# Kernel optimization log

Measured on AMD Instinct MI355X. Metric: run time of the kernel, lower is better.

Reference implementation:

```python
import jax, jax.numpy as jnp
import numpy as np

B, DIM, H, W = 1, 96, 192, 192
HEADS = 6
HD = DIM // HEADS
WIN = (8, 4)
STRIDE = (4, 2)
WH, WW = WIN
N = WH * WW
SCALE = HD ** -0.5
EPS = 1e-8

_hs = np.arange(0, H - WH + 1, STRIDE[0])
_ws = np.arange(0, W - WW + 1, STRIDE[1])
NH, NW = len(_hs), len(_ws)
HIDX = jnp.asarray(_hs[:, None] + np.arange(WH)[None, :])  # (NH, WH)
WIDX = jnp.asarray(_ws[:, None] + np.arange(WW)[None, :])  # (NW, WW)

# relative-position index table (N, N)
_co = np.stack(np.meshgrid(np.arange(WH), np.arange(WW), indexing='ij')).reshape(2, -1)
_rp = _co[:, :, None] - _co[:, None, :]
_rp[0] += WH - 1
_rp[1] += WW - 1
_rp[0] *= 2 * WW - 1
REL_IDX = jnp.asarray(_rp[0] + _rp[1])


def _clin(wr, wi, x):
    # complex 1x1 conv as channel matmul
    xr, xi = x.real, x.imag
    yr = jnp.einsum('oc,nchw->nohw', wr, xr) - jnp.einsum('oc,nchw->nohw', wi, xi)
    yi = jnp.einsum('oc,nchw->nohw', wr, xi) + jnp.einsum('oc,nchw->nohw', wi, xr)
    return jax.lax.complex(yr, yi)


def _bn(x, g, b):
    # BatchNorm2d in training mode: batch statistics, biased variance, eps=1e-5
    mu = x.mean(axis=(0, 2, 3), keepdims=True)
    var = ((x - mu) ** 2).mean(axis=(0, 2, 3), keepdims=True)
    return g[None, :, None, None] * (x - mu) * jax.lax.rsqrt(var + 1e-5) + b[None, :, None, None]


def _cbn(x, gr, br, gi, bi):
    return jax.lax.complex(_bn(x.real, gr, br), _bn(x.imag, gi, bi))


def _cgelu(x):
    mag = jnp.abs(x)
    return x * (jax.nn.gelu(mag, approximate=False) / (mag + EPS))


def _heads(t):
    # (Bn, H*D, wh, ww) -> (Bn, H, N, D)
    return t.reshape(-1, HEADS, HD, N).transpose(0, 1, 3, 2)


def reference(x_real, x_imag, qkv_wr, qkv_wi, proj_wr, proj_wi, rel,
              mlp1_wr, mlp1_wi, mlp2_wr, mlp2_wi,
              n1_gr, n1_br, n1_gi, n1_bi, n2_gr, n2_br, n2_gi, n2_bi):
    x = jax.lax.complex(x_real, x_imag)  # (B, C, H, W)

    # unfold: gather overlapping windows -> (B, C, NH, NW, WH, WW)
    xw = x[:, :, HIDX[:, None, :, None], WIDX[None, :, None, :]]
    xw = xw.transpose(0, 2, 3, 1, 4, 5).reshape(B * NH * NW, DIM, WH, WW)

    qkv = _clin(qkv_wr, qkv_wi, xw)
    q, k, v = jnp.split(qkv, 3, axis=1)
    q, k, v = _heads(q), _heads(k), _heads(v)

    attn = jnp.einsum('bhnd,bhmd->bhnm', q, jnp.conj(k)) * SCALE
    bias = rel[:, REL_IDX]  # (HEADS, N, N), real
    attn = attn + bias[None]
    mag = jnp.abs(attn)
    wsm = jax.nn.softmax(mag, axis=-1)
    attn = attn * (wsm / (mag + EPS))  # magnitude-softmax, phase preserved
    out = jnp.einsum('bhnm,bhmd->bhnd', attn, v)
    out = out.transpose(0, 1, 3, 2).reshape(-1, DIM, WH, WW)
    out = _clin(proj_wr, proj_wi, out)

    # fold: scatter-add windows back, then overlap-average
    out = out.reshape(B, NH, NW, DIM, WH, WW).transpose(0, 3, 1, 2, 4, 5)
    folded = jnp.zeros((B, DIM, H, W), jnp.complex64).at[
        :, :, HIDX[:, None, :, None], WIDX[None, :, None, :]].add(out)
    counts = jnp.zeros((H, W), jnp.float32).at[
        HIDX[:, None, :, None], WIDX[None, :, None, :]].add(1.0)
    x_ = folded / (counts + EPS)

    x = _cbn(x + x_, n1_gr, n1_br, n1_gi, n1_bi)
    m = _clin(mlp2_wr, mlp2_wi, _cgelu(_clin(mlp1_wr, mlp1_wi, x)))
    x = _cbn(x + m, n2_gr, n2_br, n2_gi, n2_bi)
    return jnp.stack([x.real, x.imag], axis=0)  # (2, B, C, H, W)


def setup_inputs() -> dict:
    key = jax.random.key(0)
    ks = jax.random.split(key, 11)
    n = lambda k, s: jax.random.normal(k, s, jnp.float32) * 0.02
    return {
        'x_real': jax.random.normal(ks[0], (B, DIM, H, W), jnp.float32),
        'x_imag': jax.random.normal(ks[1], (B, DIM, H, W), jnp.float32),
        'qkv_wr': n(ks[2], (3 * DIM, DIM)), 'qkv_wi': n(ks[3], (3 * DIM, DIM)),
        'proj_wr': n(ks[4], (DIM, DIM)), 'proj_wi': n(ks[5], (DIM, DIM)),
        'rel': n(ks[6], (HEADS, (2 * WH - 1) * (2 * WW - 1))),
        'mlp1_wr': n(ks[7], (4 * DIM, DIM)), 'mlp1_wi': n(ks[8], (4 * DIM, DIM)),
        'mlp2_wr': n(ks[9], (DIM, 4 * DIM)), 'mlp2_wi': n(ks[10], (DIM, 4 * DIM)),
        'n1_gr': jnp.ones(DIM), 'n1_br': jnp.zeros(DIM),
        'n1_gi': jnp.ones(DIM), 'n1_bi': jnp.zeros(DIM),
        'n2_gr': jnp.ones(DIM), 'n2_br': jnp.zeros(DIM),
        'n2_gi': jnp.ones(DIM), 'n2_bi': jnp.zeros(DIM),
    }
```

## Files before the change

kernel.cpp:

```cpp
#include <hip/hip_runtime.h>
#include <math.h>

#define PIX 36864
#define IMW 192
#define NWIN 4465
#define NWIN_W 95
#define NTASK (NWIN * 6)

typedef short bf16x8 __attribute__((ext_vector_type(8)));
typedef short bf16x4 __attribute__((ext_vector_type(4)));
typedef float floatx4 __attribute__((ext_vector_type(4)));

#if defined(__has_builtin)
#  if __has_builtin(__builtin_amdgcn_rcpf)
#    define RCP(x) __builtin_amdgcn_rcpf(x)
#  endif
#endif
#ifndef RCP
#  define RCP(x) (1.0f / (x))
#endif

__device__ __forceinline__ unsigned short f2bf(float f) {
    union { float f; unsigned u; } v; v.f = f;
    unsigned r = v.u + 0x7fff + ((v.u >> 16) & 1);
    return (unsigned short)(r >> 16);
}
__device__ __forceinline__ float bf2f(unsigned short b) {
    union { unsigned u; float f; } v; v.u = ((unsigned)b) << 16;
    return v.f;
}

__device__ __forceinline__ void emit3(
    const float* __restrict__ wr, const float* __restrict__ wi,
    unsigned short* __restrict__ outr, unsigned short* __restrict__ outi,
    unsigned short* __restrict__ outni, int e)
{
    outr[e] = f2bf(wr[e]);
    unsigned short b = f2bf(wi[e]);
    outi[e]  = b;
    outni[e] = b ^ 0x8000;
}

__global__ __launch_bounds__(256) void prep_kernel(
    const float* __restrict__ qwr, const float* __restrict__ qwi,
    const float* __restrict__ pwr, const float* __restrict__ pwi,
    const float* __restrict__ w2r, const float* __restrict__ w2i,
    const float* __restrict__ xr,  const float* __restrict__ xi,
    unsigned short* __restrict__ wq, unsigned short* __restrict__ wp,
    unsigned short* __restrict__ w2, float* __restrict__ ssum,
    unsigned short* __restrict__ dr, unsigned short* __restrict__ di)
{
    int blk = blockIdx.x;
    if (blk < 108)      { emit3(qwr, qwi, wq, wq + 27648, wq + 55296, blk * 256 + threadIdx.x); return; }
    if (blk < 144)      { emit3(pwr, pwi, wp, wp + 9216,  wp + 18432, (blk - 108) * 256 + threadIdx.x); return; }
    if (blk < 288)      { emit3(w2r, w2i, w2, w2 + 36864, w2 + 73728, (blk - 144) * 256 + threadIdx.x); return; }
    if (blk == 288)     { for (int j = threadIdx.x; j < 768; j += 256) ssum[j] = 0.f; return; }
    int e  = blk - 289;
    int kb = e / 144;
    int n  = (e % 144) * 256 + threadIdx.x;
    bf16x8 vr, vi;
#pragma unroll
    for (int j = 0; j < 8; ++j) {
        ((unsigned short*)&vr)[j] = f2bf(xr[(size_t)(kb * 8 + j) * PIX + n]);
        ((unsigned short*)&vi)[j] = f2bf(xi[(size_t)(kb * 8 + j) * PIX + n]);
    }
    *(bf16x8*)&dr[((size_t)kb * PIX + n) * 8] = vr;
    *(bf16x8*)&di[((size_t)kb * PIX + n) * 8] = vi;
}

template<int K, int MT, int STORE>
__global__ __launch_bounds__(256, 2) void cgemm_mfma_kernel(
    const unsigned short* __restrict__ Wr, const unsigned short* __restrict__ Wi,
    const unsigned short* __restrict__ Wni,
    const unsigned short* __restrict__ Xr, const unsigned short* __restrict__ Xi,
    unsigned short* __restrict__ Pr, unsigned short* __restrict__ Pi, int N)
{
    const int lane = threadIdx.x & 63;
    const int wave = threadIdx.x >> 6;
    const int g = lane >> 4;
    const int r = lane & 15;
    const int m0 = (blockIdx.x % MT) * 32;
    const int n0 = (blockIdx.x / MT) * 256 + wave * 64;

    floatx4 accR[2][4], accI[2][4];
#pragma unroll
    for (int t = 0; t < 2; ++t)
#pragma unroll
        for (int j = 0; j < 4; ++j) {
            accR[t][j] = (floatx4){0.f, 0.f, 0.f, 0.f};
            accI[t][j] = (floatx4){0.f, 0.f, 0.f, 0.f};
        }

    for (int kc = 0; kc < K; kc += 32) {
        bf16x8 awr[2], awi[2], awni[2];
#pragma unroll
        for (int t = 0; t < 2; ++t) {
            size_t wb = (size_t)(m0 + t * 16 + r) * K + kc + g * 8;
            awr[t]  = *(const bf16x8*)&Wr[wb];
            awi[t]  = *(const bf16x8*)&Wi[wb];
            awni[t] = *(const bf16x8*)&Wni[wb];
        }
        bf16x8 bxr[4], bxi[4];
        const size_t krow = (size_t)((kc >> 3) + g);
#pragma unroll
        for (int j = 0; j < 4; ++j) {
            size_t off = (krow * N + n0 + j * 16 + r) * 8;
            bxr[j] = *(const bf16x8*)&Xr[off];
            bxi[j] = *(const bf16x8*)&Xi[off];
        }
#pragma unroll
        for (int t = 0; t < 2; ++t)
#pragma unroll
            for (int j = 0; j < 4; ++j) {
                accR[t][j] = __builtin_amdgcn_mfma_f32_16x16x32_bf16(awr[t],  bxr[j], accR[t][j], 0, 0, 0);
                accR[t][j] = __builtin_amdgcn_mfma_f32_16x16x32_bf16(awni[t], bxi[j], accR[t][j], 0, 0, 0);
                accI[t][j] = __builtin_amdgcn_mfma_f32_16x16x32_bf16(awr[t],  bxi[j], accI[t][j], 0, 0, 0);
                accI[t][j] = __builtin_amdgcn_mfma_f32_16x16x32_bf16(awi[t],  bxr[j], accI[t][j], 0, 0, 0);
            }
    }

    if (STORE == 3) {
#pragma unroll
        for (int t = 0; t < 2; ++t)
#pragma unroll
            for (int j = 0; j < 4; ++j) {
                int col = n0 + j * 16 + r;
#pragma unroll
                for (int reg = 0; reg < 4; ++reg) {
                    int row = m0 + t * 16 + g * 4 + reg;
                    Pr[(size_t)row * N + col] = f2bf(accR[t][j][reg]);
                    Pi[(size_t)row * N + col] = f2bf(accI[t][j][reg]);
                }
            }
    } else {
#pragma unroll
        for (int t = 0; t < 2; ++t) {
            int ch0 = m0 + t * 16;
            int which = ch0 / 96;
            int hh = (ch0 % 96) / 16;
#pragma unroll
            for (int j = 0; j < 4; ++j) {
                int col = n0 + j * 16 + r;
                bf16x4 pr, pi;
#pragma unroll
                for (int reg = 0; reg < 4; ++reg) {
                    ((unsigned short*)&pr)[reg] = f2bf(accR[t][j][reg]);
                    ((unsigned short*)&pi)[reg] = f2bf(accI[t][j][reg]);
                }
                size_t sb = (((size_t)col * 3 + which) * 6 + hh) * 32;
                *(bf16x4*)&Pr[sb + g * 4]      = pr;
                *(bf16x4*)&Pr[sb + 16 + g * 4] = pi;
            }
        }
    }
}

__global__ __launch_bounds__(256) void attn_mfma_kernel(
    const unsigned short* __restrict__ qkvb,
    const float* __restrict__ rel,
    unsigned short* __restrict__ wout)
{
    __shared__ unsigned aLDS[4][32 * 36];
    __shared__ unsigned vLDS[4][32 * 17];

    const int wv   = threadIdx.x >> 6;
    const int lane = threadIdx.x & 63;
    const int lr   = lane & 15;
    const int g    = lane >> 4;

    int t = blockIdx.x * 4 + wv;
    if (t >= NTASK) t = NTASK - 1;
    const int w = t / 6, h = t % 6;
    const int nh = w / NWIN_W, nw = w % NWIN_W;
    const int r0 = nh * 4, c0 = nw * 2;
    const int slot = ((nh & 1) << 1) | (nw & 1);

    unsigned* AL = aLDS[wv];
    unsigned* VL = vLDS[wv];

    auto slotq = [&](int p, int which) -> size_t {
        int gpix = (r0 + (p >> 2)) * IMW + c0 + (p & 3);
        return ((size_t)gpix * 18 + which * 6 + h) * 32;
    };

    {
        int m = lane & 31;
        int half = lane >> 5;
        size_t sv = slotq(m, 2);
        const bf16x8 vr = *(const bf16x8*)&qkvb[sv + half * 8];
        const bf16x8 vi = *(const bf16x8*)&qkvb[sv + 16 + half * 8];
#pragma unroll
        for (int j = 0; j < 8; ++j) {
            unsigned pk = (unsigned)(unsigned short)vr[j] |
                          ((unsigned)(unsigned short)vi[j] << 16);
            VL[m * 17 + half * 8 + j] = pk;
        }
    }

    const int hoff = (g >> 1) * 16;
    const int loff = (g & 1) * 8;
    const unsigned sm = (g >= 2) ? 0x80008000u : 0u;
    bf16x8 Are[2], Aim[2], Bre[2], Bim[2];
#pragma unroll
    for (int tt = 0; tt < 2; ++tt) {
        size_t sq = slotq(tt * 16 + lr, 0);
        size_t sk = slotq(tt * 16 + lr, 1);
        Are[tt] = *(const bf16x8*)&qkvb[sq + hoff + loff];
        Aim[tt] = *(const bf16x8*)&qkvb[sq + (16 - hoff) + loff];
        Bre[tt] = *(const bf16x8*)&qkvb[sk + hoff + loff];
        bf16x8 tmp = Bre[tt];
        unsigned* u = (unsigned*)&tmp;
        u[0] ^= sm; u[1] ^= sm; u[2] ^= sm; u[3] ^= sm;
        Bim[tt] = tmp;
    }

    const floatx4 z4 = (floatx4){0.f, 0.f, 0.f, 0.f};
    floatx4 Sre[2][2], Sim[2][2];
#pragma unroll
    for (int tn = 0; tn < 2; ++tn)
#pragma unroll
        for (int tm = 0; tm < 2; ++tm) {
            Sre[tn][tm] = __builtin_amdgcn_mfma_f32_16x16x32_bf16(Are[tn], Bre[tm], z4, 0, 0, 0);
            Sim[tn][tm] = __builtin_amdgcn_mfma_f32_16x16x32_bf16(Aim[tn], Bim[tm], z4, 0, 0, 0);
        }

    const float* relh = rel + h * 105;
#pragma unroll
    for (int tn = 0; tn < 2; ++tn)
#pragma unroll
        for (int tm = 0; tm < 2; ++tm) {
            int m = tm * 16 + lr;
            int ym = m >> 2, xm = m & 3;
            int yn = tn * 4 + g;
            int bidx = (yn - ym + 7) * 7 + (3 - xm);
#pragma unroll
            for (int reg = 0; reg < 4; ++reg) {
                float re = Sre[tn][tm][reg] * 0.25f + relh[bidx + reg];
                float im = Sim[tn][tm][reg] * 0.25f;
                int n = tn * 16 + g * 4 + reg;
                AL[n * 36 + m] = (unsigned)f2bf(re) | ((unsigned)f2bf(im) << 16);
            }
        }
    __syncthreads();

    {
        const int row = lane & 31;
        const int half = lane >> 5;
        unsigned* rp = &AL[row * 36 + half * 16];
        unsigned pk[16];
        *(uint4*)&pk[0]  = *(const uint4*)&rp[0];
        *(uint4*)&pk[4]  = *(const uint4*)&rp[4];
        *(uint4*)&pk[8]  = *(const uint4*)&rp[8];
        *(uint4*)&pk[12] = *(const uint4*)&rp[12];
        float re[16], im[16], mg[16];
#pragma unroll
        for (int j = 0; j < 16; ++j) {
            union { unsigned u; float f; } a, b;
            a.u = pk[j] << 16;
            b.u = pk[j] & 0xffff0000u;
            re[j] = a.f; im[j] = b.f;
            mg[j] = sqrtf(a.f * a.f + b.f * b.f);
        }
        float mx = mg[0];
#pragma unroll
        for (int j = 1; j < 16; ++j) mx = fmaxf(mx, mg[j]);
        mx = fmaxf(mx, __shfl_xor(mx, 32, 64));
        float es[16], ss = 0.f;
#pragma unroll
        for (int j = 0; j < 16; ++j) { es[j] = __expf(mg[j] - mx); ss += es[j]; }
        ss += __shfl_xor(ss, 32, 64);
        float inv = RCP(ss);
#pragma unroll
        for (int j = 0; j < 16; ++j) {
            float f = es[j] * inv * RCP(mg[j] + 1e-8f);
            pk[j] = (unsigned)f2bf(re[j] * f) | ((unsigned)f2bf(im[j] * f) << 16);
        }
        *(uint4*)&rp[0]  = *(uint4*)&pk[0];
        *(uint4*)&rp[4]  = *(uint4*)&pk[4];
        *(uint4*)&rp[8]  = *(uint4*)&pk[8];
        *(uint4*)&rp[12] = *(uint4*)&pk[12];
    }
    __syncthreads();

    floatx4 Pre[2] = {z4, z4}, Pim[2] = {z4, z4};
#pragma unroll
    for (int kc = 0; kc < 2; ++kc) {
        bf16x8 Bpr, Bpi;
        unsigned* bpr = (unsigned*)&Bpr;
        unsigned* bpi = (unsigned*)&Bpi;
#pragma unroll
        for (int p = 0; p < 4; ++p) {
            unsigned pv = VL[(kc * 16 + g * 4 + p) * 17 + lr];
            bpr[p] = pv ^ 0x80000000u;
            bpi[p] = (pv >> 16) | (pv << 16);
        }
#pragma unroll
        for (int tn = 0; tn < 2; ++tn) {
            bf16x8 Af = *(bf16x8*)&AL[(tn * 16 + lr) * 36 + kc * 16 + g * 4];
            Pre[tn] = __builtin_amdgcn_mfma_f32_16x16x32_bf16(Af, Bpr, Pre[tn], 0, 0, 0);
            Pim[tn] = __builtin_amdgcn_mfma_f32_16x16x32_bf16(Af, Bpi, Pim[tn], 0, 0, 0);
        }
    }

#pragma unroll
    for (int tn = 0; tn < 2; ++tn)
#pragma unroll
        for (int reg = 0; reg < 4; ++reg) {
            int n = tn * 16 + g * 4 + reg;
            int gpix = (r0 + (n >> 2)) * IMW + c0 + (n & 3);
            int ch = h * 16 + lr;
            unsigned pk = (unsigned)f2bf(Pre[tn][reg]) |
                          ((unsigned)f2bf(Pim[tn][reg]) << 16);
            *(unsigned*)&wout[(((size_t)gpix * 4 + slot) * 96 + ch) * 2] = pk;
        }
}

__global__ __launch_bounds__(256) void fold_pack_kernel(
    const unsigned short* __restrict__ wout,
    unsigned short* __restrict__ dr, unsigned short* __restrict__ di)
{
    int e = blockIdx.x * 256 + threadIdx.x;
    int gpix = e / 12;
    int kb   = e % 12;
    int r = gpix / IMW, c = gpix % IMW;
    int nh0 = (r >= 7) ? ((r - 4) >> 2) : 0;
    int nh1 = min(46, r >> 2);
    int nw0 = (c >= 3) ? ((c - 2) >> 1) : 0;
    int nw1 = min(94, c >> 1);

    float accr[8] = {0,0,0,0,0,0,0,0}, acci[8] = {0,0,0,0,0,0,0,0};
    int cnt = 0;
    for (int nh = nh0; nh <= nh1; ++nh)
        for (int nw = nw0; nw <= nw1; ++nw) {
            int slot = ((nh & 1) << 1) | (nw & 1);
            const unsigned short* src = &wout[(((size_t)gpix * 4 + slot) * 96 + kb * 8) * 2];
            bf16x8 a = *(const bf16x8*)&src[0];
            bf16x8 b = *(const bf16x8*)&src[8];
#pragma unroll
            for (int j = 0; j < 4; ++j) {
                accr[j]     += bf2f((unsigned short)a[j*2]);
                acci[j]     += bf2f((unsigned short)a[j*2+1]);
                accr[4 + j] += bf2f((unsigned short)b[j*2]);
                acci[4 + j] += bf2f((unsigned short)b[j*2+1]);
            }
            ++cnt;
        }
    float invc = 1.0f / ((float)cnt + 1e-8f);
    bf16x8 pr, pi;
#pragma unroll
    for (int j = 0; j < 8; ++j) {
        ((unsigned short*)&pr)[j] = f2bf(accr[j] * invc);
        ((unsigned short*)&pi)[j] = f2bf(acci[j] * invc);
    }
    *(bf16x8*)&dr[((size_t)kb * PIX + gpix) * 8] = pr;
    *(bf16x8*)&di[((size_t)kb * PIX + gpix) * 8] = pi;
}

__device__ __forceinline__ void reduce32_commit(
    float* st, int kb, float* __restrict__ ssum)
{
#pragma unroll
    for (int v = 0; v < 32; ++v)
#pragma unroll
        for (int msk = 1; msk < 64; msk <<= 1)
            st[v] += __shfl_xor(st[v], msk, 64);
    __shared__ float red[4][32];
    const int wv = threadIdx.x >> 6;
    if ((threadIdx.x & 63) == 0)
#pragma unroll
        for (int v = 0; v < 32; ++v) red[wv][v] = st[v];
    __syncthreads();
    if (threadIdx.x < 32) {
        float s = red[0][threadIdx.x] + red[1][threadIdx.x] +
                  red[2][threadIdx.x] + red[3][threadIdx.x];
        int ch = kb * 8 + (threadIdx.x >> 2);
        int stat = threadIdx.x & 3;
        int base = (stat < 2) ? ch : 96 + ch;
        atomicAdd(&ssum[base * 2 + (stat & 1)], s);
    }
}

__global__ __launch_bounds__(256) void combine_pack_kernel(
    const float* __restrict__ xr, const float* __restrict__ xi,
    const unsigned short* __restrict__ pr, const unsigned short* __restrict__ pi,
    unsigned short* __restrict__ dr, unsigned short* __restrict__ di,
    float* __restrict__ ssum)
{
    const int kb = blockIdx.x / 36;
    const int pb = blockIdx.x % 36;
    const int p0 = pb * 1024;
    float st[32];
#pragma unroll
    for (int v = 0; v < 32; ++v) st[v] = 0.f;

#pragma unroll
    for (int it = 0; it < 4; ++it) {
        int p = p0 + it * 256 + threadIdx.x;
        bf16x8 vr, vi;
#pragma unroll
        for (int ch = 0; ch < 8; ++ch) {
            int c = kb * 8 + ch;
            float a = xr[(size_t)c * PIX + p] + bf2f(pr[(size_t)c * PIX + p]);
            float b = xi[(size_t)c * PIX + p] + bf2f(pi[(size_t)c * PIX + p]);
            ((unsigned short*)&vr)[ch] = f2bf(a);
            ((unsigned short*)&vi)[ch] = f2bf(b);
            st[ch * 4 + 0] += a; st[ch * 4 + 1] += a * a;
            st[ch * 4 + 2] += b; st[ch * 4 + 3] += b * b;
        }
        *(bf16x8*)&dr[((size_t)kb * PIX + p) * 8] = vr;
        *(bf16x8*)&di[((size_t)kb * PIX + p) * 8] = vi;
    }
    reduce32_commit(st, kb, ssum);
}

__global__ __launch_bounds__(256) void scale_w_kernel(
    const float* __restrict__ w1r, const float* __restrict__ w1i,
    const float* __restrict__ gr, const float* __restrict__ br,
    const float* __restrict__ gi, const float* __restrict__ bi,
    const float* __restrict__ ssum1,
    unsigned short* __restrict__ W0, unsigned short* __restrict__ W1,
    unsigned short* __restrict__ W2, unsigned short* __restrict__ W3,
    float* __restrict__ biasR, float* __restrict__ biasI)
{
    const float invn = 1.0f / (float)PIX;
    int blk = blockIdx.x;
    if (blk < 576) {
        int e = blk * 256 + threadIdx.x;
        int mat = e / 36864;
        int idx = e % 36864;
        int k = idx % 96;
        float mr = ssum1[k * 2] * invn;
        float a_r = gr[k] * rsqrtf(ssum1[k * 2 + 1] * invn - mr * mr + 1e-5f);
        float mi = ssum1[(96 + k) * 2] * invn;
        float a_i = gi[k] * rsqrtf(ssum1[(96 + k) * 2 + 1] * invn - mi * mi + 1e-5f);
        float wr = w1r[idx], wi = w1i[idx];
        float v = (mat == 0) ? wr * a_r : (mat == 1) ? -wi * a_i
                : (mat == 2) ? wr * a_i : wi * a_r;
        unsigned short* dst = (mat == 0) ? W0 : (mat == 1) ? W1 : (mat == 2) ? W2 : W3;
        dst[idx] = f2bf(v);
    } else {
        int o = (blk - 576) * 256 + threadIdx.x;
        if (o >= 768) return;
        int isI = o >= 384;
        int oo = o % 384;
        float acc = 0.f;
        for (int k = 0; k < 96; ++k) {
            float mr = ssum1[k * 2] * invn;
            float a_r = gr[k] * rsqrtf(ssum1[k * 2 + 1] * invn - mr * mr + 1e-5f);
            float c_r = br[k] - a_r * mr;
            float mi = ssum1[(96 + k) * 2] * invn;
            float a_i = gi[k] * rsqrtf(ssum1[(96 + k) * 2 + 1] * invn - mi * mi + 1e-5f);
            float c_i = bi[k] - a_i * mi;
            float wr = w1r[oo * 96 + k], wi = w1i[oo * 96 + k];
            acc += isI ? (wr * c_i + wi * c_r) : (wr * c_r - wi * c_i);
        }
        (isI ? biasI : biasR)[oo] = acc;
    }
}

__global__ __launch_bounds__(256, 2) void mlp1bn_kernel(
    const unsigned short* __restrict__ W0, const unsigned short* __restrict__ W1,
    const unsigned short* __restrict__ W2, const unsigned short* __restrict__ W3,
    const float* __restrict__ biasR, const float* __restrict__ biasI,
    const unsigned short* __restrict__ Xr, const unsigned short* __restrict__ Xi,
    unsigned short* __restrict__ Pr, unsigned short* __restrict__ Pi, int N)
{
    const int lane = threadIdx.x & 63;
    const int wave = threadIdx.x >> 6;
    const int g = lane >> 4;
    const int r = lane & 15;
    const int m0 = (blockIdx.x % 12) * 32;
    const int n0 = (blockIdx.x / 12) * 256 + wave * 64;
    const int K = 96;

    floatx4 accR[2][4], accI[2][4];
#pragma unroll
    for (int t = 0; t < 2; ++t)
#pragma unroll
        for (int j = 0; j < 4; ++j) {
            accR[t][j] = (floatx4){0.f, 0.f, 0.f, 0.f};
            accI[t][j] = (floatx4){0.f, 0.f, 0.f, 0.f};
        }

    for (int kc = 0; kc < K; kc += 32) {
        bf16x8 a0[2], a1[2], a2[2], a3[2];
#pragma unroll
        for (int t = 0; t < 2; ++t) {
            size_t wb = (size_t)(m0 + t * 16 + r) * K + kc + g * 8;
            a0[t] = *(const bf16x8*)&W0[wb];
            a1[t] = *(const bf16x8*)&W1[wb];
            a2[t] = *(const bf16x8*)&W2[wb];
            a3[t] = *(const bf16x8*)&W3[wb];
        }
        bf16x8 bxr[4], bxi[4];
        const size_t krow = (size_t)((kc >> 3) + g);
#pragma unroll
        for (int j = 0; j < 4; ++j) {
            size_t off = (krow * N + n0 + j * 16 + r) * 8;
            bxr[j] = *(const bf16x8*)&Xr[off];
            bxi[j] = *(const bf16x8*)&Xi[off];
        }
#pragma unroll
        for (int t = 0; t < 2; ++t)
#pragma unroll
            for (int j = 0; j < 4; ++j) {
                accR[t][j] = __builtin_amdgcn_mfma_f32_16x16x32_bf16(a0[t], bxr[j], accR[t][j], 0, 0, 0);
                accR[t][j] = __builtin_amdgcn_mfma_f32_16x16x32_bf16(a1[t], bxi[j], accR[t][j], 0, 0, 0);
                accI[t][j] = __builtin_amdgcn_mfma_f32_16x16x32_bf16(a2[t], bxi[j], accI[t][j], 0, 0, 0);
                accI[t][j] = __builtin_amdgcn_mfma_f32_16x16x32_bf16(a3[t], bxr[j], accI[t][j], 0, 0, 0);
            }
    }

#pragma unroll
    for (int t = 0; t < 2; ++t) {
        float bR[4], bI[4];
#pragma unroll
        for (int reg = 0; reg < 4; ++reg) {
            int row = m0 + t * 16 + g * 4 + reg;
            bR[reg] = biasR[row];
            bI[reg] = biasI[row];
        }
#pragma unroll
        for (int j = 0; j < 4; ++j) {
            int col = n0 + j * 16 + r;
            size_t rowblk = (size_t)((m0 + t * 16 + g * 4) >> 3);
            int sub = (g & 1) * 4;
            bf16x4 pr, pi;
#pragma unroll
            for (int reg = 0; reg < 4; ++reg) {
                float a = accR[t][j][reg] + bR[reg];
                float b = accI[t][j][reg] + bI[reg];
                float mag = sqrtf(a * a + b * b);
                float f = (0.5f + 0.5f * erff(mag * 0.70710678118654752f)) * mag * RCP(mag + 1e-8f);
                ((unsigned short*)&pr)[reg] = f2bf(a * f);
                ((unsigned short*)&pi)[reg] = f2bf(b * f);
            }
            *(bf16x4*)&Pr[(rowblk * N + col) * 8 + sub] = pr;
            *(bf16x4*)&Pi[(rowblk * N + col) * 8 + sub] = pi;
        }
    }
}

__global__ __launch_bounds__(256) void addbn_kernel(
    const unsigned short* __restrict__ dr, const unsigned short* __restrict__ di,
    const float* __restrict__ ssum1,
    const float* __restrict__ gr, const float* __restrict__ br,
    const float* __restrict__ gi, const float* __restrict__ bi,
    const unsigned short* __restrict__ mr_, const unsigned short* __restrict__ mi_,
    unsigned short* __restrict__ s2r, unsigned short* __restrict__ s2i,
    float* __restrict__ ssum2)
{
    const int kb = blockIdx.x / 36;
    const int pb = blockIdx.x % 36;
    const int p0 = pb * 1024;
    const float invn = 1.0f / (float)PIX;

    float ar[8], cr[8], ai[8], ci[8];
#pragma unroll
    for (int ch = 0; ch < 8; ++ch) {
        int c = kb * 8 + ch;
        float mr = ssum1[c * 2] * invn;
        ar[ch] = gr[c] * rsqrtf(ssum1[c * 2 + 1] * invn - mr * mr + 1e-5f);
        cr[ch] = br[c] - ar[ch] * mr;
        float mi = ssum1[(96 + c) * 2] * invn;
        ai[ch] = gi[c] * rsqrtf(ssum1[(96 + c) * 2 + 1] * invn - mi * mi + 1e-5f);
        ci[ch] = bi[c] - ai[ch] * mi;
    }

    float st[32];
#pragma unroll
    for (int v = 0; v < 32; ++v) st[v] = 0.f;

#pragma unroll
    for (int it = 0; it < 4; ++it) {
        int p = p0 + it * 256 + threadIdx.x;
        bf16x8 s1r = *(const bf16x8*)&dr[((size_t)kb * PIX + p) * 8];
        bf16x8 s1i = *(const bf16x8*)&di[((size_t)kb * PIX + p) * 8];
#pragma unroll
        for (int ch = 0; ch < 8; ++ch) {
            int c = kb * 8 + ch;
            float vr = bf2f(mr_[(size_t)c * PIX + p]) + ar[ch] * bf2f((unsigned short)s1r[ch]) + cr[ch];
            float vi = bf2f(mi_[(size_t)c * PIX + p]) + ai[ch] * bf2f((unsigned short)s1i[ch]) + ci[ch];
            s2r[(size_t)c * PIX + p] = f2bf(vr);
            s2i[(size_t)c * PIX + p] = f2bf(vi);
            st[ch * 4 + 0] += vr; st[ch * 4 + 1] += vr * vr;
            st[ch * 4 + 2] += vi; st[ch * 4 + 3] += vi * vi;
        }
    }
    reduce32_commit(st, kb, ssum2);
}

__global__ __launch_bounds__(256) void bn_apply_kernel(
    const unsigned short* __restrict__ s2r, const unsigned short* __restrict__ s2i,
    const float* __restrict__ gr, const float* __restrict__ br,
    const float* __restrict__ gi, const float* __restrict__ bi,
    const float* __restrict__ ssum2,
    float* __restrict__ outr, float* __restrict__ outi)
{
    int e = blockIdx.x * 256 + threadIdx.x;
    if (e >= 96 * PIX) return;
    int ch = e / PIX;
    const float invn = 1.0f / (float)PIX;
    float mr = ssum2[ch * 2] * invn;
    float isr = rsqrtf(ssum2[ch * 2 + 1] * invn - mr * mr + 1e-5f);
    float mi = ssum2[(96 + ch) * 2] * invn;
    float isi = rsqrtf(ssum2[(96 + ch) * 2 + 1] * invn - mi * mi + 1e-5f);
    outr[e] = gr[ch] * (bf2f(s2r[e]) - mr) * isr + br[ch];
    outi[e] = gi[ch] * (bf2f(s2i[e]) - mi) * isi + bi[ch];
}

extern "C" void kernel_launch(void* const* d_in, const int* in_sizes, int n_in,
                              void* d_out, int out_size, void* d_ws, size_t ws_size,
                              hipStream_t stream)
{
    const float* x_r     = (const float*)d_in[0];
    const float* x_i     = (const float*)d_in[1];
    const float* qkv_wr  = (const float*)d_in[2];
    const float* qkv_wi  = (const float*)d_in[3];
    const float* proj_wr = (const float*)d_in[4];
    const float* proj_wi = (const float*)d_in[5];
    const float* rel     = (const float*)d_in[6];
    const float* mlp1_wr = (const float*)d_in[7];
    const float* mlp1_wi = (const float*)d_in[8];
    const float* mlp2_wr = (const float*)d_in[9];
    const float* mlp2_wi = (const float*)d_in[10];
    const float* n1_gr   = (const float*)d_in[11];
    const float* n1_br   = (const float*)d_in[12];
    const float* n1_gi   = (const float*)d_in[13];
    const float* n1_bi   = (const float*)d_in[14];
    const float* n2_gr   = (const float*)d_in[15];
    const float* n2_br   = (const float*)d_in[16];
    const float* n2_gi   = (const float*)d_in[17];
    const float* n2_bi   = (const float*)d_in[18];

    const size_t P = PIX;
    char* base = (char*)d_ws;

    unsigned short* Dr = (unsigned short*)base;
    unsigned short* Di = Dr + 96 * P;
    char* R = (char*)(Di + 96 * P);
    unsigned short* qkvb = (unsigned short*)R;
    unsigned short* wout = qkvb + 576 * P;
    unsigned short* pm_r = (unsigned short*)R;
    unsigned short* pm_i = pm_r + 96 * P;
    unsigned short* hid_r = pm_i + 96 * P;
    unsigned short* hid_i = hid_r + 384 * P;
    unsigned short* Wb = wout + (size_t)P * 4 * 96 * 2;

    unsigned short* wq = Wb;
    unsigned short* wp = Wb + 82944;
    unsigned short* w2 = Wb + 110592;
    unsigned short* W1s = Wb + 221184;
    float* biasR = (float*)(Wb + 368640);
    float* biasI = biasR + 384;
    float* ssum1 = biasI + 384;
    float* ssum2 = ssum1 + 384;
    unsigned short* s2r = (unsigned short*)(ssum2 + 384);
    unsigned short* s2i = s2r + 96 * P;

    float* out_r = (float*)d_out;
    float* out_i = out_r + 96 * P;

    dim3 blk(256);

    prep_kernel<<<dim3(2017), blk, 0, stream>>>(
        qkv_wr, qkv_wi, proj_wr, proj_wi, mlp2_wr, mlp2_wi, x_r, x_i,
        wq, wp, w2, ssum1, Dr, Di);
    cgemm_mfma_kernel<96, 9, 2><<<dim3(9 * 144), blk, 0, stream>>>(
        wq, wq + 27648, wq + 55296, Dr, Di, qkvb, nullptr, PIX);
    attn_mfma_kernel<<<dim3((NTASK + 3) / 4), blk, 0, stream>>>(qkvb, rel, wout);
    fold_pack_kernel<<<dim3(1728), blk, 0, stream>>>(wout, Dr, Di);
    cgemm_mfma_kernel<96, 3, 3><<<dim3(3 * 144), blk, 0, stream>>>(
        wp, wp + 9216, wp + 18432, Dr, Di, pm_r, pm_i, PIX);
    combine_pack_kernel<<<dim3(432), blk, 0, stream>>>(x_r, x_i, pm_r, pm_i, Dr, Di, ssum1);
    scale_w_kernel<<<dim3(579), blk, 0, stream>>>(
        mlp1_wr, mlp1_wi, n1_gr, n1_br, n1_gi, n1_bi, ssum1,
        W1s, W1s + 36864, W1s + 73728, W1s + 110592, biasR, biasI);
    mlp1bn_kernel<<<dim3(12 * 144), blk, 0, stream>>>(
        W1s, W1s + 36864, W1s + 73728, W1s + 110592, biasR, biasI,
        Dr, Di, hid_r, hid_i, PIX);
    cgemm_mfma_kernel<384, 3, 3><<<dim3(3 * 144), blk, 0, stream>>>(
        w2, w2 + 36864, w2 + 73728, hid_r, hid_i, pm_r, pm_i, PIX);
    addbn_kernel<<<dim3(432), blk, 0, stream>>>(Dr, Di, ssum1,
        n1_gr, n1_br, n1_gi, n1_bi, pm_r, pm_i, s2r, s2i, ssum2);
    bn_apply_kernel<<<dim3(13824), blk, 0, stream>>>(s2r, s2i,
        n2_gr, n2_br, n2_gi, n2_bi, ssum2, out_r, out_i);
}
```

Baseline: 344.0 us.

## Pack bf16 pairs with perm, interleave V storage, drop attention block barriers

Adds a pk_bf helper that rounds two floats and packs them into one 32-bit word with a single byte-permute, and uses it everywhere bf16 pairs are emitted. This replaces the per-element shift/or packing. The QKV GEMM now writes V slots already interleaved as (re,im) pairs, so the attention kernel copies them straight into LDS with vector loads instead of repacking per element. The __syncthreads in the attention kernel are replaced with compiler-only memory fences, on the basis that each wave uses its own LDS region. This relies on intra-wave LDS ordering and changes the V layout contract between the two kernels.

Result: slower. 361.6 us (+5.1%).

```diff
diff --git a/kernel.cpp b/kernel.cpp
--- a/kernel.cpp
+++ b/kernel.cpp
@@ -29,6 +29,13 @@
     union { unsigned u; float f; } v; v.u = ((unsigned)b) << 16;
     return v.f;
 }
+__device__ __forceinline__ unsigned bfround(float f) {
+    union { float f; unsigned u; } v; v.f = f;
+    return v.u + 0x7fff + ((v.u >> 16) & 1);
+}
+__device__ __forceinline__ unsigned pk_bf(float lo, float hi) {
+    return __builtin_amdgcn_perm(bfround(hi), bfround(lo), 0x07060302u);
+}
 
 __device__ __forceinline__ void emit3(
     const float* __restrict__ wr, const float* __restrict__ wi,
@@ -58,14 +65,20 @@
     int e  = blk - 289;
     int kb = e / 144;
     int n  = (e % 144) * 256 + threadIdx.x;
-    bf16x8 vr, vi;
+    float fr[8], fi[8];
 #pragma unroll
     for (int j = 0; j < 8; ++j) {
-        ((unsigned short*)&vr)[j] = f2bf(xr[(size_t)(kb * 8 + j) * PIX + n]);
-        ((unsigned short*)&vi)[j] = f2bf(xi[(size_t)(kb * 8 + j) * PIX + n]);
-    }
-    *(bf16x8*)&dr[((size_t)kb * PIX + n) * 8] = vr;
-    *(bf16x8*)&di[((size_t)kb * PIX + n) * 8] = vi;
+        fr[j] = xr[(size_t)(kb * 8 + j) * PIX + n];
+        fi[j] = xi[(size_t)(kb * 8 + j) * PIX + n];
+    }
+    unsigned vr[4], vi[4];
+#pragma unroll
+    for (int j = 0; j < 4; ++j) {
+        vr[j] = pk_bf(fr[j * 2], fr[j * 2 + 1]);
+        vi[j] = pk_bf(fi[j * 2], fi[j * 2 + 1]);
+    }
+    *(uint4*)&dr[((size_t)kb * PIX + n) * 8] = *(uint4*)vr;
+    *(uint4*)&di[((size_t)kb * PIX + n) * 8] = *(uint4*)vi;
 }
 
 template<int K, int MT, int STORE>
@@ -141,15 +154,22 @@
 #pragma unroll
             for (int j = 0; j < 4; ++j) {
                 int col = n0 + j * 16 + r;
-                bf16x4 pr, pi;
-#pragma unroll
-                for (int reg = 0; reg < 4; ++reg) {
-                    ((unsigned short*)&pr)[reg] = f2bf(accR[t][j][reg]);
-                    ((unsigned short*)&pi)[reg] = f2bf(accI[t][j][reg]);
+                size_t sb = (((size_t)col * 3 + which) * 6 + hh) * 32;
+                if (which == 2) {
+                    unsigned vv[4];
+#pragma unroll
+                    for (int reg = 0; reg < 4; ++reg)
+                        vv[reg] = pk_bf(accR[t][j][reg], accI[t][j][reg]);
+                    *(uint4*)&Pr[sb + g * 8] = *(uint4*)vv;
+                } else {
+                    uint2 pr, pi;
+                    pr.x = pk_bf(accR[t][j][0], accR[t][j][1]);
+                    pr.y = pk_bf(accR[t][j][2], accR[t][j][3]);
+                    pi.x = pk_bf(accI[t][j][0], accI[t][j][1]);
+                    pi.y = pk_bf(accI[t][j][2], accI[t][j][3]);
+                    *(uint2*)&Pr[sb + g * 4]      = pr;
+                    *(uint2*)&Pr[sb + 16 + g * 4] = pi;
                 }
-                size_t sb = (((size_t)col * 3 + which) * 6 + hh) * 32;
-                *(bf16x4*)&Pr[sb + g * 4]      = pr;
-                *(bf16x4*)&Pr[sb + 16 + g * 4] = pi;
             }
         }
     }
@@ -187,15 +207,13 @@
         int m = lane & 31;
         int half = lane >> 5;
         size_t sv = slotq(m, 2);
-        const bf16x8 vr = *(const bf16x8*)&qkvb[sv + half * 8];
-        const bf16x8 vi = *(const bf16x8*)&qkvb[sv + 16 + half * 8];
-#pragma unroll
-        for (int j = 0; j < 8; ++j) {
-            unsigned pk = (unsigned)(unsigned short)vr[j] |
-                          ((unsigned)(unsigned short)vi[j] << 16);
-            VL[m * 17 + half * 8 + j] = pk;
-        }
-    }
+        uint4 u0 = *(const uint4*)&qkvb[sv + half * 16];
+        uint4 u1 = *(const uint4*)&qkvb[sv + half * 16 + 8];
+        unsigned* dst = &VL[m * 17 + half * 8];
+        dst[0] = u0.x; dst[1] = u0.y; dst[2] = u0.z; dst[3] = u0.w;
+        dst[4] = u1.x; dst[5] = u1.y; dst[6] = u1.z; dst[7] = u1.w;
+    }
+    __asm__ volatile("" ::: "memory");
 
     const int hoff = (g >> 1) * 16;
     const int loff = (g & 1) * 8;
@@ -238,10 +256,10 @@
                 float re = Sre[tn][tm][reg] * 0.25f + relh[bidx + reg];
                 float im = Sim[tn][tm][reg] * 0.25f;
                 int n = tn * 16 + g * 4 + reg;
-                AL[n * 36 + m] = (unsigned)f2bf(re) | ((unsigned)f2bf(im) << 16);
+                AL[n * 36 + m] = pk_bf(re, im);
             }
         }
-    __syncthreads();
+    __asm__ volatile("" ::: "memory");
 
     {
         const int row = lane & 31;
@@ -273,14 +291,14 @@
 #pragma unroll
         for (int j = 0; j < 16; ++j) {
             float f = es[j] * inv * RCP(mg[j] + 1e-8f);
-            pk[j] = (unsigned)f2bf(re[j] * f) | ((unsigned)f2bf(im[j] * f) << 16);
+            pk[j] = pk_bf(re[j] * f, im[j] * f);
         }
         *(uint4*)&rp[0]  = *(uint4*)&pk[0];
         *(uint4*)&rp[4]  = *(uint4*)&pk[4];
         *(uint4*)&rp[8]  = *(uint4*)&pk[8];
         *(uint4*)&rp[12] = *(uint4*)&pk[12];
     }
-    __syncthreads();
+    __asm__ volatile("" ::: "memory");
 
     floatx4 Pre[2] = {z4, z4}, Pim[2] = {z4, z4};
 #pragma unroll
@@ -309,9 +327,8 @@
             int n = tn * 16 + g * 4 + reg;
             int gpix = (r0 + (n >> 2)) * IMW + c0 + (n & 3);
             int ch = h * 16 + lr;
-            unsigned pk = (unsigned)f2bf(Pre[tn][reg]) |
-                          ((unsigned)f2bf(Pim[tn][reg]) << 16);
-            *(unsigned*)&wout[(((size_t)gpix * 4 + slot) * 96 + ch) * 2] = pk;
+            *(unsigned*)&wout[(((size_t)gpix * 4 + slot) * 96 + ch) * 2] =
+                pk_bf(Pre[tn][reg], Pim[tn][reg]);
         }
 }
 
@@ -346,14 +363,14 @@
             ++cnt;
         }
     float invc = 1.0f / ((float)cnt + 1e-8f);
-    bf16x8 pr, pi;
-#pragma unroll
-    for (int j = 0; j < 8; ++j) {
-        ((unsigned short*)&pr)[j] = f2bf(accr[j] * invc);
-        ((unsigned short*)&pi)[j] = f2bf(acci[j] * invc);
-    }
-    *(bf16x8*)&dr[((size_t)kb * PIX + gpix) * 8] = pr;
-    *(bf16x8*)&di[((size_t)kb * PIX + gpix) * 8] = pi;
+    unsigned pr[4], pi[4];
+#pragma unroll
+    for (int j = 0; j < 4; ++j) {
+        pr[j] = pk_bf(accr[j * 2] * invc, accr[j * 2 + 1] * invc);
+        pi[j] = pk_bf(acci[j * 2] * invc, acci[j * 2 + 1] * invc);
+    }
+    *(uint4*)&dr[((size_t)kb * PIX + gpix) * 8] = *(uint4*)pr;
+    *(uint4*)&di[((size_t)kb * PIX + gpix) * 8] = *(uint4*)pi;
 }
 
 __device__ __forceinline__ void reduce32_commit(
@@ -396,19 +413,23 @@
 #pragma unroll
     for (int it = 0; it < 4; ++it) {
         int p = p0 + it * 256 + threadIdx.x;
-        bf16x8 vr, vi;
+        float a_[8], b_[8];
 #pragma unroll
         for (int ch = 0; ch < 8; ++ch) {
             int c = kb * 8 + ch;
-            float a = xr[(size_t)c * PIX + p] + bf2f(pr[(size_t)c * PIX + p]);
-            float b = xi[(size_t)c * PIX + p] + bf2f(pi[(size_t)c * PIX + p]);
-            ((unsigned short*)&vr)[ch] = f2bf(a);
-            ((unsigned short*)&vi)[ch] = f2bf(b);
-            st[ch * 4 + 0] += a; st[ch * 4 + 1] += a * a;
-            st[ch * 4 + 2] += b; st[ch * 4 + 3] += b * b;
-        }
-        *(bf16x8*)&dr[((size_t)kb * PIX + p) * 8] = vr;
-        *(bf16x8*)&di[((size_t)kb * PIX + p) * 8] = vi;
+            a_[ch] = xr[(size_t)c * PIX + p] + bf2f(pr[(size_t)c * PIX + p]);
+            b_[ch] = xi[(size_t)c * PIX + p] + bf2f(pi[(size_t)c * PIX + p]);
+            st[ch * 4 + 0] += a_[ch]; st[ch * 4 + 1] += a_[ch] * a_[ch];
+            st[ch * 4 + 2] += b_[ch]; st[ch * 4 + 3] += b_[ch] * b_[ch];
+        }
+        unsigned vr[4], vi[4];
+#pragma unroll
+        for (int j = 0; j < 4; ++j) {
+            vr[j] = pk_bf(a_[j * 2], a_[j * 2 + 1]);
+            vi[j] = pk_bf(b_[j * 2], b_[j * 2 + 1]);
+        }
+        *(uint4*)&dr[((size_t)kb * PIX + p) * 8] = *(uint4*)vr;
+        *(uint4*)&di[((size_t)kb * PIX + p) * 8] = *(uint4*)vi;
     }
     reduce32_commit(st, kb, ssum);
 }
@@ -525,18 +546,21 @@
             int col = n0 + j * 16 + r;
             size_t rowblk = (size_t)((m0 + t * 16 + g * 4) >> 3);
             int sub = (g & 1) * 4;
-            bf16x4 pr, pi;
+            float cr[4], ci[4];
 #pragma unroll
             for (int reg = 0; reg < 4; ++reg) {
                 float a = accR[t][j][reg] + bR[reg];
                 float b = accI[t][j][reg] + bI[reg];
                 float mag = sqrtf(a * a + b * b);
                 float f = (0.5f + 0.5f * erff(mag * 0.70710678118654752f)) * mag * RCP(mag + 1e-8f);
-                ((unsigned short*)&pr)[reg] = f2bf(a * f);
-                ((unsigned short*)&pi)[reg] = f2bf(b * f);
+                cr[reg] = a * f;
+                ci[reg] = b * f;
             }
-            *(bf16x4*)&Pr[(rowblk * N + col) * 8 + sub] = pr;
-            *(bf16x4*)&Pi[(rowblk * N + col) * 8 + sub] = pi;
+            uint2 pr, pi;
+            pr.x = pk_bf(cr[0], cr[1]); pr.y = pk_bf(cr[2], cr[3]);
+            pi.x = pk_bf(ci[0], ci[1]); pi.y = pk_bf(ci[2], ci[3]);
+            *(uint2*)&Pr[(rowblk * N + col) * 8 + sub] = pr;
+            *(uint2*)&Pi[(rowblk * N + col) * 8 + sub] = pi;
         }
     }
 }
```
